# Kernel tuning notes

Hardware: AMD Instinct MI355X
Metric: run time of the kernel (lower is better)

## Reference

```python
import jax, jax.numpy as jnp
import numpy as np
from jax import lax

B, T, D = 4, 1024, 1024
H = 16
HD = D // H
MIN_K, MAX_K = 3, 9
KS = (3, 5, 7, 9)  # candidate odd kernel sizes


def setup_inputs() -> dict:
    key = jax.random.key(0)
    ks = jax.random.split(key, 16)
    s = 0.02
    inp = {
        "x": jax.random.normal(ks[0], (B, T, D), jnp.float32),
        "Wq": jax.random.normal(ks[1], (D, D), jnp.float32) * s,
        "bq": jnp.zeros((D,), jnp.float32),
        "Wk": jax.random.normal(ks[2], (D, D), jnp.float32) * s,
        "bk": jnp.zeros((D,), jnp.float32),
        "Wv": jax.random.normal(ks[3], (D, D), jnp.float32) * s,
        "bv": jnp.zeros((D,), jnp.float32),
        # per-head Conv1d weights (H, out_ch=HD, in_ch=HD, MAX_K) and biases (H, HD)
        "conv_w": jax.random.normal(ks[4], (H, HD, HD, MAX_K), jnp.float32) * s,
        "conv_b": jax.random.normal(ks[5], (H, HD), jnp.float32) * s,
        # kernel_proj: Linear(1,16) -> ReLU -> Linear(16,1), stored as (in,out)
        "kp_w1": jax.random.normal(ks[6], (1, 16), jnp.float32) * 0.5,
        "kp_b1": jnp.zeros((16,), jnp.float32),
        "kp_w2": jax.random.normal(ks[7], (16, 1), jnp.float32) * 0.5,
        "kp_b2": jnp.zeros((1,), jnp.float32),
        "fc_w": jax.random.normal(ks[8], (D, D), jnp.float32) * s,
        "fc_b": jnp.zeros((D,), jnp.float32),
        "ln_g": jnp.ones((D,), jnp.float32),
        "ln_b": jnp.zeros((D,), jnp.float32),
    }
    return inp


def reference(x, Wq, bq, Wk, bk, Wv, bv, conv_w, conv_b,
              kp_w1, kp_b1, kp_w2, kp_b2, fc_w, fc_b, ln_g, ln_b):
    scale = HD ** -0.5
    q = (x @ Wq + bq).reshape(B, T, H, HD).transpose(0, 2, 1, 3)  # (B,H,T,HD)
    k = (x @ Wk + bk).reshape(B, T, H, HD).transpose(0, 2, 1, 3)
    v = (x @ Wv + bv).reshape(B, T, H, HD).transpose(0, 2, 1, 3)

    attn = jax.nn.softmax(jnp.einsum('bhqd,bhkd->bhqk', q, k) * scale, axis=-1)

    # head importance -> dynamic kernel size per head
    importance = attn.mean(axis=(-2, -1)).mean(axis=0)  # (H,)
    imp_norm = (importance - importance.min()) / (importance.max() - importance.min() + 1e-6)
    hmid = jax.nn.relu(imp_norm[:, None] @ kp_w1 + kp_b1)  # (H,16)
    frac = jax.nn.sigmoid((hmid @ kp_w2 + kp_b2)[:, 0])    # (H,)
    kv = jnp.round(MIN_K + frac * (MAX_K - MIN_K)).astype(jnp.int32)
    kv = kv + (1 - kv % 2)                                 # force odd
    kv = jnp.clip(kv, MIN_K, MAX_K)
    k_idx = jnp.clip((kv - MIN_K) // 2, 0, len(KS) - 1)    # (H,) candidate index

    out = jnp.einsum('bhqk,bhkd->bhqd', attn, v)           # (B,H,T,HD)
    out_c = out.transpose(0, 1, 3, 2).reshape(B, H * HD, T)  # NCH grouped layout

    center = MAX_K // 2
    cands = []
    for kk in KS:
        half = kk // 2
        w = conv_w[:, :, :, center - half:center + half + 1].reshape(H * HD, HD, kk)
        y = lax.conv_general_dilated(out_c, w, (1,), 'VALID',
                                     dimension_numbers=('NCH', 'OIH', 'NCH'),
                                     feature_group_count=H)
        y = y + conv_b.reshape(1, H * HD, 1)
        # smart edge-replication pad of conv OUTPUT back to length T
        y = jnp.pad(y, ((0, 0), (0, 0), (half, kk - 1 - half)), mode='edge')
        cands.append(y)
    cands = jnp.stack(cands).reshape(len(KS), B, H, HD, T)  # (K,B,H,HD,T)

    onehot = jax.nn.one_hot(k_idx, len(KS), dtype=cands.dtype)  # (H,K)
    sel = jnp.einsum('kbhdt,hk->bhdt', cands, onehot)           # (B,H,HD,T)
    out_cat = sel.transpose(0, 3, 1, 2).reshape(B, T, D)

    proj = out_cat @ fc_w + fc_b
    y = proj + x
    mu = y.mean(axis=-1, keepdims=True)
    var = ((y - mu) ** 2).mean(axis=-1, keepdims=True)
    return (y - mu) / jnp.sqrt(var + 1e-5) * ln_g + ln_b
```

## Files before the change

kernel.cpp:

```cpp
#include <hip/hip_runtime.h>
#include <math.h>

constexpr int Bn = 4, Tn = 1024, Dn = 1024, Hn = 16, HDn = 64;

typedef __attribute__((ext_vector_type(8))) short short8;
typedef __attribute__((ext_vector_type(4))) float floatx4;
typedef __attribute__((ext_vector_type(4))) unsigned short ushort4v;

static __device__ __forceinline__ unsigned short f2bf(float f) {
  union { float f; unsigned int u; } v; v.f = f;
  unsigned int u = v.u;
  unsigned int r = (u + 0x7fffu + ((u >> 16) & 1u)) >> 16;
  return (unsigned short)r;
}

static __device__ __forceinline__ unsigned short f2bf_fast(float f) {
  union { float f; unsigned int u; } v; v.f = f;
  return (unsigned short)((v.u + 0x8000u) >> 16);
}

static __device__ __forceinline__ void gload_lds16(const void* g, void* l) {
  __builtin_amdgcn_global_load_lds(
      (const __attribute__((address_space(1))) unsigned int*)g,
      (__attribute__((address_space(3))) unsigned int*)l, 16, 0, 0);
}


__global__ __launch_bounds__(256) void prep_misc(
    const float* __restrict__ X, unsigned short* __restrict__ Xb,
    const float* __restrict__ conv_w, unsigned short* __restrict__ Wc)
{
  if (blockIdx.x < 4096) {
    int i = (blockIdx.x * 256 + threadIdx.x) * 4;
    float4 v = *(const float4*)(X + i);
    ushort4v o;
    o.x = f2bf(v.x); o.y = f2bf(v.y); o.z = f2bf(v.z); o.w = f2bf(v.w);
    *(ushort4v*)(Xb + i) = o;
  } else {
    int idx = (blockIdx.x - 4096) * 256 + threadIdx.x;
    int i = idx & 63;
    int o = (idx >> 6) & 63;
    int j = (idx >> 12) % 7;
    int h = idx / (7 * 4096);
    Wc[idx] = f2bf(conv_w[(((size_t)(h * 64 + o) * 64 + i) * 9) + 1 + j]);
  }
}

__global__ __launch_bounds__(256) void transpose_cast(
    const float* __restrict__ W0, const float* __restrict__ W1,
    const float* __restrict__ W2, const float* __restrict__ W3,
    unsigned short* __restrict__ O0, unsigned short* __restrict__ O1,
    unsigned short* __restrict__ O2, unsigned short* __restrict__ O3)
{
  const int z = blockIdx.z;
  const float* W = (z == 0) ? W0 : (z == 1) ? W1 : (z == 2) ? W2 : W3;
  unsigned short* O = (z == 0) ? O0 : (z == 1) ? O1 : (z == 2) ? O2 : O3;
  __shared__ float tile[64][65];
  const int tid = threadIdx.x;
  const int c0 = blockIdx.x * 64, r0 = blockIdx.y * 64;
  for (int i = tid; i < 4096; i += 256) {
    int r = i >> 6, c = i & 63;
    tile[r][c] = W[(size_t)(r0 + r) * 1024 + c0 + c];
  }
  __syncthreads();
  for (int i = tid; i < 4096; i += 256) {
    int r = i >> 6, c = i & 63;
    O[(size_t)(c0 + r) * 1024 + r0 + c] = f2bf(tile[c][r]);
  }
}

__global__ __launch_bounds__(256) void gemm_qkv_mfma(
    const unsigned short* __restrict__ Ab,
    const unsigned short* __restrict__ WqT, const unsigned short* __restrict__ WkT,
    const unsigned short* __restrict__ WvT,
    const float* __restrict__ bq, const float* __restrict__ bk, const float* __restrict__ bv,
    unsigned short* __restrict__ Qb, unsigned short* __restrict__ Kb,
    unsigned short* __restrict__ Vtb)
{
  __shared__ unsigned short As[128 * 64];
  __shared__ unsigned short Bs[128 * 64];
  const int tid = threadIdx.x;
  const int lane = tid & 63;
  const int ln = lane & 15, g = lane >> 4;
  const int wave = tid >> 6;
  const int wm = (wave >> 1) * 64, wn = (wave & 1) * 64;
  const int m0 = blockIdx.y * 128;
  const int ng = blockIdx.x * 128;
  const int which = ng >> 10;
  const int n0 = ng & 1023;
  const unsigned short* Wt = (which == 0) ? WqT : (which == 1) ? WkT : WvT;
  const float* bia = (which == 0) ? bq : (which == 1) ? bk : bv;

  const unsigned short* aSrc[4]; unsigned short* aDst[4];
  const unsigned short* bSrc[4]; unsigned short* bDst[4];
  #pragma unroll
  for (int it = 0; it < 4; ++it) {
    int L = it * 256 + tid;
    int r = L >> 3, sc = L & 7;
    int c = sc ^ (r & 7);
    aSrc[it] = Ab + (size_t)(m0 + r) * 1024 + c * 8;
    aDst[it] = As + L * 8;
    bSrc[it] = Wt + (size_t)(n0 + r) * 1024 + c * 8;
    bDst[it] = Bs + L * 8;
  }

  floatx4 acc[4][4];
  #pragma unroll
  for (int mt = 0; mt < 4; ++mt)
    #pragma unroll
    for (int nt = 0; nt < 4; ++nt) acc[mt][nt] = (floatx4)0.f;

  for (int k0 = 0; k0 < 1024; k0 += 64) {
    __syncthreads();
    #pragma unroll
    for (int it = 0; it < 4; ++it) {
      gload_lds16(aSrc[it] + k0, aDst[it]);
      gload_lds16(bSrc[it] + k0, bDst[it]);
    }
    __syncthreads();
    #pragma unroll
    for (int s = 0; s < 2; ++s) {
      short8 af[4], bf[4];
      #pragma unroll
      for (int mt = 0; mt < 4; ++mt) {
        int R = wm + mt * 16 + ln;
        int ch = (s * 4 + g) ^ (R & 7);
        af[mt] = *(const short8*)&As[(R * 8 + ch) * 8];
      }
      #pragma unroll
      for (int nt = 0; nt < 4; ++nt) {
        int R = wn + nt * 16 + ln;
        int ch = (s * 4 + g) ^ (R & 7);
        bf[nt] = *(const short8*)&Bs[(R * 8 + ch) * 8];
      }
      #pragma unroll
      for (int mt = 0; mt < 4; ++mt)
        #pragma unroll
        for (int nt = 0; nt < 4; ++nt)
          acc[mt][nt] = __builtin_amdgcn_mfma_f32_16x16x32_bf16(af[mt], bf[nt], acc[mt][nt], 0, 0, 0);
    }
  }

  const int b = m0 >> 10;
  const int tbase = m0 & 1023;
  #pragma unroll
  for (int nt = 0; nt < 4; ++nt) {
    int nl = wn + nt * 16 + ln;
    float bv_ = bia[n0 + nl];
    int h = (n0 + nl) >> 6, hd = (n0 + nl) & 63;
    #pragma unroll
    for (int mt = 0; mt < 4; ++mt) {
      int t = tbase + wm + mt * 16 + g * 4;
      if (which < 2) {
        unsigned short* Out = (which == 0) ? Qb : Kb;
        size_t base = (((size_t)b * Hn + h) * Tn + t) * HDn + hd;
        #pragma unroll
        for (int r = 0; r < 4; ++r)
          Out[base + (size_t)r * HDn] = f2bf(acc[mt][nt][r] + bv_);
      } else {
        ushort4v o;
        #pragma unroll
        for (int r = 0; r < 4; ++r) o[r] = f2bf(acc[mt][nt][r] + bv_);
        *(ushort4v*)(Vtb + (((size_t)b * Hn + h) * HDn + hd) * Tn + t) = o;
      }
    }
  }
}

__global__ __launch_bounds__(256) void gemm_fc_mfma(
    const unsigned short* __restrict__ Ab, const unsigned short* __restrict__ WT,
    const float* __restrict__ bia, float* __restrict__ PR)
{
  __shared__ unsigned short As[128 * 64];
  __shared__ unsigned short Bs[128 * 64];
  const int tid = threadIdx.x;
  const int lane = tid & 63;
  const int ln = lane & 15, g = lane >> 4;
  const int wave = tid >> 6;
  const int wm = (wave >> 1) * 64, wn = (wave & 1) * 64;
  const int m0 = blockIdx.y * 128;
  const int n0 = blockIdx.x * 128;

  const unsigned short* aSrc[4]; unsigned short* aDst[4];
  const unsigned short* bSrc[4]; unsigned short* bDst[4];
  #pragma unroll
  for (int it = 0; it < 4; ++it) {
    int L = it * 256 + tid;
    int r = L >> 3, sc = L & 7;
    int c = sc ^ (r & 7);
    aSrc[it] = Ab + (size_t)(m0 + r) * 1024 + c * 8;
    aDst[it] = As + L * 8;
    bSrc[it] = WT + (size_t)(n0 + r) * 1024 + c * 8;
    bDst[it] = Bs + L * 8;
  }

  floatx4 acc[4][4];
  #pragma unroll
  for (int mt = 0; mt < 4; ++mt)
    #pragma unroll
    for (int nt = 0; nt < 4; ++nt) acc[mt][nt] = (floatx4)0.f;

  for (int k0 = 0; k0 < 1024; k0 += 64) {
    __syncthreads();
    #pragma unroll
    for (int it = 0; it < 4; ++it) {
      gload_lds16(aSrc[it] + k0, aDst[it]);
      gload_lds16(bSrc[it] + k0, bDst[it]);
    }
    __syncthreads();
    #pragma unroll
    for (int s = 0; s < 2; ++s) {
      short8 af[4], bf[4];
      #pragma unroll
      for (int mt = 0; mt < 4; ++mt) {
        int R = wm + mt * 16 + ln;
        int ch = (s * 4 + g) ^ (R & 7);
        af[mt] = *(const short8*)&As[(R * 8 + ch) * 8];
      }
      #pragma unroll
      for (int nt = 0; nt < 4; ++nt) {
        int R = wn + nt * 16 + ln;
        int ch = (s * 4 + g) ^ (R & 7);
        bf[nt] = *(const short8*)&Bs[(R * 8 + ch) * 8];
      }
      #pragma unroll
      for (int mt = 0; mt < 4; ++mt)
        #pragma unroll
        for (int nt = 0; nt < 4; ++nt)
          acc[mt][nt] = __builtin_amdgcn_mfma_f32_16x16x32_bf16(af[mt], bf[nt], acc[mt][nt], 0, 0, 0);
    }
  }

  #pragma unroll
  for (int nt = 0; nt < 4; ++nt) {
    int n = n0 + wn + nt * 16 + ln;
    float bv_ = bia[n];
    #pragma unroll
    for (int mt = 0; mt < 4; ++mt) {
      int m = m0 + wm + mt * 16 + g * 4;
      float* base = PR + (size_t)m * Dn + n;
      #pragma unroll
      for (int r = 0; r < 4; ++r) base[(size_t)r * Dn] = acc[mt][nt][r] + bv_;
    }
  }
}

__global__ __launch_bounds__(256) void attn_mfma(
    const unsigned short* __restrict__ Qb, const unsigned short* __restrict__ Kb,
    const unsigned short* __restrict__ Vtb, unsigned short* __restrict__ AO)
{
  __shared__ unsigned short Ks[64 * 64];
  __shared__ unsigned short Vts[64 * 64];
  __shared__ unsigned short Ps[64 * 72];

  const int bh = blockIdx.y;
  const int q0 = blockIdx.x * 64;
  const int tid = threadIdx.x;
  const int lane = tid & 63;
  const int ln = lane & 15;
  const int g  = lane >> 4;
  const int wq = (tid >> 6) * 16;

  const unsigned short* Kp  = Kb  + (size_t)bh * Tn * HDn;
  const unsigned short* Vtp = Vtb + (size_t)bh * HDn * Tn;

  const unsigned short* Qrow = Qb + ((size_t)bh * Tn + q0 + wq + ln) * HDn;
  short8 qa0 = *(const short8*)(Qrow + g * 8);
  short8 qa1 = *(const short8*)(Qrow + 32 + g * 8);

  const unsigned short* kSrc[2]; unsigned short* kDst[2];
  const unsigned short* vSrc[2]; unsigned short* vDst[2];
  #pragma unroll
  for (int it = 0; it < 2; ++it) {
    int L = it * 256 + tid;
    int r = L >> 3, sc = L & 7;
    int c = sc ^ (r & 7);
    kSrc[it] = Kp + (size_t)r * HDn + c * 8;
    kDst[it] = Ks + L * 8;
    vSrc[it] = Vtp + (size_t)r * Tn + c * 8;
    vDst[it] = Vts + L * 8;
  }

  floatx4 o[4];
  #pragma unroll
  for (int dt = 0; dt < 4; ++dt) o[dt] = (floatx4)0.f;
  float l[4] = {0.f, 0.f, 0.f, 0.f};

  constexpr float CEXP = 0.18033688011112042f;

  for (int kt = 0; kt < Tn; kt += 64) {
    __syncthreads();
    #pragma unroll
    for (int it = 0; it < 2; ++it) {
      gload_lds16(kSrc[it] + (size_t)kt * HDn, kDst[it]);
      gload_lds16(vSrc[it] + kt, vDst[it]);
    }
    __syncthreads();

    floatx4 s[4];
    #pragma unroll
    for (int nt = 0; nt < 4; ++nt) {
      int R = nt * 16 + ln;
      int ch0 = g ^ (ln & 7), ch1 = (4 + g) ^ (ln & 7);
      short8 kb0 = *(const short8*)&Ks[(R * 8 + ch0) * 8];
      short8 kb1 = *(const short8*)&Ks[(R * 8 + ch1) * 8];
      s[nt] = (floatx4)0.f;
      s[nt] = __builtin_amdgcn_mfma_f32_16x16x32_bf16(qa0, kb0, s[nt], 0, 0, 0);
      s[nt] = __builtin_amdgcn_mfma_f32_16x16x32_bf16(qa1, kb1, s[nt], 0, 0, 0);
    }

    #pragma unroll
    for (int r = 0; r < 4; ++r) {
      #pragma unroll
      for (int nt = 0; nt < 4; ++nt) {
        float pv = __builtin_amdgcn_exp2f(s[nt][r] * CEXP);
        l[r] += pv;
        Ps[(wq + g * 4 + r) * 72 + nt * 16 + ln] = f2bf_fast(pv);
      }
    }

    short8 pa0 = *(const short8*)&Ps[(wq + ln) * 72 + g * 8];
    short8 pa1 = *(const short8*)&Ps[(wq + ln) * 72 + 32 + g * 8];

    #pragma unroll
    for (int dt = 0; dt < 4; ++dt) {
      int R = dt * 16 + ln;
      int ch0 = g ^ (ln & 7), ch1 = (4 + g) ^ (ln & 7);
      short8 vb0 = *(const short8*)&Vts[(R * 8 + ch0) * 8];
      short8 vb1 = *(const short8*)&Vts[(R * 8 + ch1) * 8];
      o[dt] = __builtin_amdgcn_mfma_f32_16x16x32_bf16(pa0, vb0, o[dt], 0, 0, 0);
      o[dt] = __builtin_amdgcn_mfma_f32_16x16x32_bf16(pa1, vb1, o[dt], 0, 0, 0);
    }
  }

  float inv[4];
  #pragma unroll
  for (int r = 0; r < 4; ++r) {
    float rs = l[r];
    rs += __shfl_xor(rs, 1);
    rs += __shfl_xor(rs, 2);
    rs += __shfl_xor(rs, 4);
    rs += __shfl_xor(rs, 8);
    inv[r] = 1.f / rs;
  }
  unsigned short* Op = AO + ((size_t)bh * Tn + q0 + wq) * HDn;
  #pragma unroll
  for (int dt = 0; dt < 4; ++dt)
    #pragma unroll
    for (int r = 0; r < 4; ++r)
      Op[(size_t)(g * 4 + r) * HDn + dt * 16 + ln] = f2bf(o[dt][r] * inv[r]);
}

__global__ __launch_bounds__(256) void conv_mfma(
    const unsigned short* __restrict__ Xb, const unsigned short* __restrict__ Wc,
    const float* __restrict__ conv_b, unsigned short* __restrict__ CO)
{
  __shared__ unsigned short Wl[7 * 32 * 64];
  __shared__ unsigned short Xs[134 * 64];
  const int tid = threadIdx.x;
  const int lane = tid & 63;
  const int ln = lane & 15, g = lane >> 4;
  const int wave = tid >> 6;
  const int wm = wave * 32;
  const int t0 = blockIdx.x * 128;
  const int o0 = blockIdx.y * 32;
  const int bh = blockIdx.z;
  const int b = bh >> 4, h = bh & 15;
  const unsigned short* Xp = Xb + (size_t)bh * Tn * HDn;
  const unsigned short* Wp = Wc + ((size_t)h * 7 * 64 + o0) * 64;

  #pragma unroll
  for (int it = 0; it < 7; ++it) {
    int L = it * 256 + tid;
    int row = L >> 3, sc = L & 7;
    int c = sc ^ (row & 7);
    int j = row >> 5, ol = row & 31;
    gload_lds16(Wp + ((size_t)j * 64 + ol) * 64 + c * 8, Wl + L * 8);
  }
  #pragma unroll
  for (int it = 0; it < 5; ++it) {
    int L = it * 256 + tid;
    if (L < 134 * 8) {
      int lr = L >> 3, sc = L & 7;
      int c = sc ^ (lr & 7);
      int gr = min(max(t0 - 3 + lr, 0), Tn - 1);
      gload_lds16(Xp + (size_t)gr * HDn + c * 8, Xs + L * 8);
    }
  }
  __syncthreads();

  floatx4 acc[2][2];
  #pragma unroll
  for (int mt = 0; mt < 2; ++mt)
    #pragma unroll
    for (int nt = 0; nt < 2; ++nt) acc[mt][nt] = (floatx4)0.f;

  int tb[2];
  #pragma unroll
  for (int mt = 0; mt < 2; ++mt)
    tb[mt] = min(max(t0 + wm + mt * 16 + ln, 3), Tn - 4) - t0;

  #pragma unroll
  for (int j = 0; j < 7; ++j) {
    #pragma unroll
    for (int s = 0; s < 2; ++s) {
      short8 af[2], bf[2];
      #pragma unroll
      for (int mt = 0; mt < 2; ++mt) {
        int lr = tb[mt] + j;
        int ch = (s * 4 + g) ^ (lr & 7);
        af[mt] = *(const short8*)&Xs[lr * 64 + ch * 8];
      }
      #pragma unroll
      for (int nt = 0; nt < 2; ++nt) {
        int row = j * 32 + nt * 16 + ln;
        int ch = (s * 4 + g) ^ (row & 7);
        bf[nt] = *(const short8*)&Wl[row * 64 + ch * 8];
      }
      #pragma unroll
      for (int mt = 0; mt < 2; ++mt)
        #pragma unroll
        for (int nt = 0; nt < 2; ++nt)
          acc[mt][nt] = __builtin_amdgcn_mfma_f32_16x16x32_bf16(af[mt], bf[nt], acc[mt][nt], 0, 0, 0);
    }
  }

  #pragma unroll
  for (int nt = 0; nt < 2; ++nt) {
    int o = o0 + nt * 16 + ln;
    float bias = conv_b[(h << 6) + o];
    #pragma unroll
    for (int mt = 0; mt < 2; ++mt) {
      int t = t0 + wm + mt * 16 + g * 4;
      #pragma unroll
      for (int r = 0; r < 4; ++r)
        CO[((size_t)b * Tn + t + r) * Dn + (h << 6) + o] = f2bf(acc[mt][nt][r] + bias);
    }
  }
}

__global__ __launch_bounds__(256) void res_ln(
    const float* __restrict__ P, const float* __restrict__ Xin,
    const float* __restrict__ g, const float* __restrict__ be,
    float* __restrict__ Out)
{
  const int r = blockIdx.x;
  const int tid = threadIdx.x;
  const int c = tid * 4;
  float4 pv = *(const float4*)(P + (size_t)r * Dn + c);
  float4 xv = *(const float4*)(Xin + (size_t)r * Dn + c);
  float v0 = pv.x + xv.x, v1 = pv.y + xv.y, v2 = pv.z + xv.z, v3 = pv.w + xv.w;
  float s = v0 + v1 + v2 + v3;
  float s2 = v0 * v0 + v1 * v1 + v2 * v2 + v3 * v3;
  #pragma unroll
  for (int off = 32; off > 0; off >>= 1) {
    s += __shfl_down(s, off);
    s2 += __shfl_down(s2, off);
  }
  __shared__ float rs[4], rs2[4];
  __shared__ float smu, srstd;
  const int wid = tid >> 6;
  if ((tid & 63) == 0) { rs[wid] = s; rs2[wid] = s2; }
  __syncthreads();
  if (tid == 0) {
    float S = rs[0] + rs[1] + rs[2] + rs[3];
    float S2 = rs2[0] + rs2[1] + rs2[2] + rs2[3];
    float mu = S * (1.f / Dn);
    float var = S2 * (1.f / Dn) - mu * mu;
    smu = mu;
    srstd = rsqrtf(var + 1e-5f);
  }
  __syncthreads();
  float mu = smu, rstd = srstd;
  float4 gv = *(const float4*)(g + c);
  float4 bv = *(const float4*)(be + c);
  float4 ov;
  ov.x = (v0 - mu) * rstd * gv.x + bv.x;
  ov.y = (v1 - mu) * rstd * gv.y + bv.y;
  ov.z = (v2 - mu) * rstd * gv.z + bv.z;
  ov.w = (v3 - mu) * rstd * gv.w + bv.w;
  *(float4*)(Out + (size_t)r * Dn + c) = ov;
}

extern "C" void kernel_launch(void* const* d_in, const int* in_sizes, int n_in,
                              void* d_out, int out_size, void* d_ws, size_t ws_size,
                              hipStream_t stream) {
  const float* x      = (const float*)d_in[0];
  const float* Wq     = (const float*)d_in[1];
  const float* bq     = (const float*)d_in[2];
  const float* Wk     = (const float*)d_in[3];
  const float* bk     = (const float*)d_in[4];
  const float* Wv     = (const float*)d_in[5];
  const float* bv     = (const float*)d_in[6];
  const float* conv_w = (const float*)d_in[7];
  const float* conv_b = (const float*)d_in[8];
  const float* fc_w   = (const float*)d_in[13];
  const float* fc_b   = (const float*)d_in[14];
  const float* ln_g   = (const float*)d_in[15];
  const float* ln_b   = (const float*)d_in[16];
  float* out = (float*)d_out;

  unsigned char* w8 = (unsigned char*)d_ws;
  const size_t MB = 1024 * 1024;
  unsigned short* Xb  = (unsigned short*)(w8);
  unsigned short* WqT = (unsigned short*)(w8 + 8 * MB);
  unsigned short* WkT = (unsigned short*)(w8 + 10 * MB);
  unsigned short* WvT = (unsigned short*)(w8 + 12 * MB);
  unsigned short* fcT = (unsigned short*)(w8 + 14 * MB);
  unsigned short* Qb  = (unsigned short*)(w8 + 16 * MB);
  unsigned short* Kb  = (unsigned short*)(w8 + 24 * MB);
  unsigned short* Vtb = (unsigned short*)(w8 + 32 * MB);
  unsigned short* AO  = (unsigned short*)(w8 + 40 * MB);
  unsigned short* Wc  = (unsigned short*)(w8 + 48 * MB);
  unsigned short* CO  = (unsigned short*)(w8);
  float* PR           = (float*)(w8 + 16 * MB);

  prep_misc<<<dim3(4096 + 1792), 256, 0, stream>>>(x, Xb, conv_w, Wc);
  transpose_cast<<<dim3(16, 16, 4), 256, 0, stream>>>(Wq, Wk, Wv, fc_w, WqT, WkT, WvT, fcT);
  gemm_qkv_mfma<<<dim3(24, 32), 256, 0, stream>>>(Xb, WqT, WkT, WvT, bq, bk, bv, Qb, Kb, Vtb);
  attn_mfma<<<dim3(16, 64), 256, 0, stream>>>(Qb, Kb, Vtb, AO);
  conv_mfma<<<dim3(8, 2, 64), 256, 0, stream>>>(AO, Wc, conv_b, CO);
  gemm_fc_mfma<<<dim3(8, 32), 256, 0, stream>>>(CO, fcT, fc_b, PR);
  res_ln<<<dim3(Bn * Tn), 256, 0, stream>>>(PR, x, ln_g, ln_b, out);
}
```

Measured before the change: 231.5 us.

## Merge prep kernels, store fc output as bf16, widen attention blocks to 128 queries

Folds the weight transpose-cast into the input-prep kernel so there is one fewer launch. Stores the fc GEMM output as bf16 instead of fp32 to halve that intermediate's traffic, at the cost of extra rounding before the residual and layernorm. Doubles the attention block to 512 threads covering 128 queries, so each K/V tile loaded into LDS is shared by twice as many query rows. This halves the grid and each thread now issues only one K and one V load per tile.

```diff
diff --git a/kernel.cpp b/kernel.cpp
--- a/kernel.cpp
+++ b/kernel.cpp
@@ -14,6 +14,12 @@
   return (unsigned short)r;
 }
 
+static __device__ __forceinline__ float bf2f(unsigned short s) {
+  union { unsigned int u; float f; } v;
+  v.u = ((unsigned int)s) << 16;
+  return v.f;
+}
+
 static __device__ __forceinline__ unsigned short f2bf_fast(float f) {
   union { float f; unsigned int u; } v; v.f = f;
   return (unsigned short)((v.u + 0x8000u) >> 16);
@@ -26,46 +32,46 @@
 }
 
 
-__global__ __launch_bounds__(256) void prep_misc(
+__global__ __launch_bounds__(256) void prep_all(
     const float* __restrict__ X, unsigned short* __restrict__ Xb,
-    const float* __restrict__ conv_w, unsigned short* __restrict__ Wc)
+    const float* __restrict__ conv_w, unsigned short* __restrict__ Wc,
+    const float* __restrict__ W0, const float* __restrict__ W1,
+    const float* __restrict__ W2, const float* __restrict__ W3,
+    unsigned short* __restrict__ O0, unsigned short* __restrict__ O1,
+    unsigned short* __restrict__ O2, unsigned short* __restrict__ O3)
 {
+  const int tid = threadIdx.x;
   if (blockIdx.x < 4096) {
-    int i = (blockIdx.x * 256 + threadIdx.x) * 4;
+    int i = (blockIdx.x * 256 + tid) * 4;
     float4 v = *(const float4*)(X + i);
     ushort4v o;
     o.x = f2bf(v.x); o.y = f2bf(v.y); o.z = f2bf(v.z); o.w = f2bf(v.w);
     *(ushort4v*)(Xb + i) = o;
-  } else {
-    int idx = (blockIdx.x - 4096) * 256 + threadIdx.x;
+  } else if (blockIdx.x < 5888) {
+    int idx = (blockIdx.x - 4096) * 256 + tid;
     int i = idx & 63;
     int o = (idx >> 6) & 63;
     int j = (idx >> 12) % 7;
     int h = idx / (7 * 4096);
     Wc[idx] = f2bf(conv_w[(((size_t)(h * 64 + o) * 64 + i) * 9) + 1 + j]);
-  }
-}
-
-__global__ __launch_bounds__(256) void transpose_cast(
-    const float* __restrict__ W0, const float* __restrict__ W1,
-    const float* __restrict__ W2, const float* __restrict__ W3,
-    unsigned short* __restrict__ O0, unsigned short* __restrict__ O1,
-    unsigned short* __restrict__ O2, unsigned short* __restrict__ O3)
-{
-  const int z = blockIdx.z;
-  const float* W = (z == 0) ? W0 : (z == 1) ? W1 : (z == 2) ? W2 : W3;
-  unsigned short* O = (z == 0) ? O0 : (z == 1) ? O1 : (z == 2) ? O2 : O3;
-  __shared__ float tile[64][65];
-  const int tid = threadIdx.x;
-  const int c0 = blockIdx.x * 64, r0 = blockIdx.y * 64;
-  for (int i = tid; i < 4096; i += 256) {
-    int r = i >> 6, c = i & 63;
-    tile[r][c] = W[(size_t)(r0 + r) * 1024 + c0 + c];
-  }
-  __syncthreads();
-  for (int i = tid; i < 4096; i += 256) {
-    int r = i >> 6, c = i & 63;
-    O[(size_t)(c0 + r) * 1024 + r0 + c] = f2bf(tile[c][r]);
+  } else {
+    int bid = blockIdx.x - 5888;
+    int z = bid >> 8;
+    int rem = bid & 255;
+    int cx = rem & 15, ry = rem >> 4;
+    const float* W = (z == 0) ? W0 : (z == 1) ? W1 : (z == 2) ? W2 : W3;
+    unsigned short* O = (z == 0) ? O0 : (z == 1) ? O1 : (z == 2) ? O2 : O3;
+    __shared__ float tile[64][65];
+    const int c0 = cx * 64, r0 = ry * 64;
+    for (int i = tid; i < 4096; i += 256) {
+      int r = i >> 6, c = i & 63;
+      tile[r][c] = W[(size_t)(r0 + r) * 1024 + c0 + c];
+    }
+    __syncthreads();
+    for (int i = tid; i < 4096; i += 256) {
+      int r = i >> 6, c = i & 63;
+      O[(size_t)(c0 + r) * 1024 + r0 + c] = f2bf(tile[c][r]);
+    }
   }
 }
 
@@ -169,7 +175,7 @@
 
 __global__ __launch_bounds__(256) void gemm_fc_mfma(
     const unsigned short* __restrict__ Ab, const unsigned short* __restrict__ WT,
-    const float* __restrict__ bia, float* __restrict__ PR)
+    const float* __restrict__ bia, unsigned short* __restrict__ PRb)
 {
   __shared__ unsigned short As[128 * 64];
   __shared__ unsigned short Bs[128 * 64];
@@ -238,23 +244,23 @@
     #pragma unroll
     for (int mt = 0; mt < 4; ++mt) {
       int m = m0 + wm + mt * 16 + g * 4;
-      float* base = PR + (size_t)m * Dn + n;
-      #pragma unroll
-      for (int r = 0; r < 4; ++r) base[(size_t)r * Dn] = acc[mt][nt][r] + bv_;
-    }
-  }
-}
-
-__global__ __launch_bounds__(256) void attn_mfma(
+      unsigned short* base = PRb + (size_t)m * Dn + n;
+      #pragma unroll
+      for (int r = 0; r < 4; ++r) base[(size_t)r * Dn] = f2bf(acc[mt][nt][r] + bv_);
+    }
+  }
+}
+
+__global__ __launch_bounds__(512) void attn_mfma(
     const unsigned short* __restrict__ Qb, const unsigned short* __restrict__ Kb,
     const unsigned short* __restrict__ Vtb, unsigned short* __restrict__ AO)
 {
   __shared__ unsigned short Ks[64 * 64];
   __shared__ unsigned short Vts[64 * 64];
-  __shared__ unsigned short Ps[64 * 72];
+  __shared__ unsigned short Ps[128 * 72];
 
   const int bh = blockIdx.y;
-  const int q0 = blockIdx.x * 64;
+  const int q0 = blockIdx.x * 128;
   const int tid = threadIdx.x;
   const int lane = tid & 63;
   const int ln = lane & 15;
@@ -268,18 +274,12 @@
   short8 qa0 = *(const short8*)(Qrow + g * 8);
   short8 qa1 = *(const short8*)(Qrow + 32 + g * 8);
 
-  const unsigned short* kSrc[2]; unsigned short* kDst[2];
-  const unsigned short* vSrc[2]; unsigned short* vDst[2];
-  #pragma unroll
-  for (int it = 0; it < 2; ++it) {
-    int L = it * 256 + tid;
-    int r = L >> 3, sc = L & 7;
-    int c = sc ^ (r & 7);
-    kSrc[it] = Kp + (size_t)r * HDn + c * 8;
-    kDst[it] = Ks + L * 8;
-    vSrc[it] = Vtp + (size_t)r * Tn + c * 8;
-    vDst[it] = Vts + L * 8;
-  }
+  const int r_ = tid >> 3, sc_ = tid & 7;
+  const int c_ = sc_ ^ (r_ & 7);
+  const unsigned short* kSrc = Kp + (size_t)r_ * HDn + c_ * 8;
+  unsigned short* kDst = Ks + tid * 8;
+  const unsigned short* vSrc = Vtp + (size_t)r_ * Tn + c_ * 8;
+  unsigned short* vDst = Vts + tid * 8;
 
   floatx4 o[4];
   #pragma unroll
@@ -290,11 +290,8 @@
 
   for (int kt = 0; kt < Tn; kt += 64) {
     __syncthreads();
-    #pragma unroll
-    for (int it = 0; it < 2; ++it) {
-      gload_lds16(kSrc[it] + (size_t)kt * HDn, kDst[it]);
-      gload_lds16(vSrc[it] + kt, vDst[it]);
-    }
+    gload_lds16(kSrc + (size_t)kt * HDn, kDst);
+    gload_lds16(vSrc + kt, vDst);
     __syncthreads();
 
     floatx4 s[4];
@@ -440,16 +437,17 @@
 }
 
 __global__ __launch_bounds__(256) void res_ln(
-    const float* __restrict__ P, const float* __restrict__ Xin,
+    const unsigned short* __restrict__ Pb, const float* __restrict__ Xin,
     const float* __restrict__ g, const float* __restrict__ be,
     float* __restrict__ Out)
 {
   const int r = blockIdx.x;
   const int tid = threadIdx.x;
   const int c = tid * 4;
-  float4 pv = *(const float4*)(P + (size_t)r * Dn + c);
+  ushort4v pv4 = *(const ushort4v*)(Pb + (size_t)r * Dn + c);
   float4 xv = *(const float4*)(Xin + (size_t)r * Dn + c);
-  float v0 = pv.x + xv.x, v1 = pv.y + xv.y, v2 = pv.z + xv.z, v3 = pv.w + xv.w;
+  float v0 = bf2f(pv4.x) + xv.x, v1 = bf2f(pv4.y) + xv.y;
+  float v2 = bf2f(pv4.z) + xv.z, v3 = bf2f(pv4.w) + xv.w;
   float s = v0 + v1 + v2 + v3;
   float s2 = v0 * v0 + v1 * v1 + v2 * v2 + v3 * v3;
   #pragma unroll
@@ -513,13 +511,13 @@
   unsigned short* AO  = (unsigned short*)(w8 + 40 * MB);
   unsigned short* Wc  = (unsigned short*)(w8 + 48 * MB);
   unsigned short* CO  = (unsigned short*)(w8);
-  float* PR           = (float*)(w8 + 16 * MB);
-
-  prep_misc<<<dim3(4096 + 1792), 256, 0, stream>>>(x, Xb, conv_w, Wc);
-  transpose_cast<<<dim3(16, 16, 4), 256, 0, stream>>>(Wq, Wk, Wv, fc_w, WqT, WkT, WvT, fcT);
+  unsigned short* PRb = (unsigned short*)(w8 + 16 * MB);
+
+  prep_all<<<dim3(6912), 256, 0, stream>>>(x, Xb, conv_w, Wc,
+                                           Wq, Wk, Wv, fc_w, WqT, WkT, WvT, fcT);
   gemm_qkv_mfma<<<dim3(24, 32), 256, 0, stream>>>(Xb, WqT, WkT, WvT, bq, bk, bv, Qb, Kb, Vtb);
-  attn_mfma<<<dim3(16, 64), 256, 0, stream>>>(Qb, Kb, Vtb, AO);
+  attn_mfma<<<dim3(8, 64), 512, 0, stream>>>(Qb, Kb, Vtb, AO);
   conv_mfma<<<dim3(8, 2, 64), 256, 0, stream>>>(AO, Wc, conv_b, CO);
-  gemm_fc_mfma<<<dim3(8, 32), 256, 0, stream>>>(CO, fcT, fc_b, PR);
-  res_ln<<<dim3(Bn * Tn), 256, 0, stream>>>(PR, x, ln_g, ln_b, out);
-}
+  gemm_fc_mfma<<<dim3(8, 32), 256, 0, stream>>>(CO, fcT, fc_b, PRb);
+  res_ln<<<dim3(Bn * Tn), 256, 0, stream>>>(PRb, x, ln_g, ln_b, out);
+}
```

New measurement: 221.6 us. 4.3% less time.
